# Kernel tuning notes

Hardware: AMD Instinct MI355X
Metric: run time of the kernel (lower is better)

Reference implementation:

```python
import jax, jax.numpy as jnp
import numpy as np

B, S, D, H = 4, 2048, 1024, 16
DH = D // H


def setup_inputs() -> dict:
    key = jax.random.key(0)
    ks = jax.random.split(key, 5)
    scale = 0.02
    return {
        "in_features": jax.random.normal(ks[0], (B, S, D), dtype=jnp.float32),
        "Wq": jax.random.normal(ks[1], (D, D), dtype=jnp.float32) * scale,
        "Wk": jax.random.normal(ks[2], (D, D), dtype=jnp.float32) * scale,
        "Wv": jax.random.normal(ks[3], (D, D), dtype=jnp.float32) * scale,
        "Wo": jax.random.normal(ks[4], (D, D), dtype=jnp.float32) * scale,
    }


def reference(in_features, Wq, Wk, Wv, Wo):
    x = in_features  # [B, S, D]
    # projections: einsum '... s d_in, d_model d_in -> ... s d_model'  == x @ W.T
    q = jnp.einsum('bsd,md->bsm', x, Wq)
    k = jnp.einsum('bsd,md->bsm', x, Wk)
    v = jnp.einsum('bsd,md->bsm', x, Wv)
    # split heads: [B, H, S, DH]
    q = q.reshape(B, S, H, DH).transpose(0, 2, 1, 3)
    k = k.reshape(B, S, H, DH).transpose(0, 2, 1, 3)
    v = v.reshape(B, S, H, DH).transpose(0, 2, 1, 3)
    scale = 1.0 / jnp.sqrt(jnp.asarray(DH, dtype=q.dtype))
    scores = jnp.einsum('bhqd,bhkd->bhqk', q, k) * scale  # [B, H, S, S]
    causal = jnp.tril(jnp.ones((S, S), dtype=bool))
    scores = jnp.where(causal[None, None, :, :], scores, -jnp.inf)
    attn = jax.nn.softmax(scores, axis=-1)
    out = jnp.einsum('bhqk,bhkd->bhqd', attn, v)  # [B, H, S, DH]
    out = out.transpose(0, 2, 1, 3).reshape(B, S, D)
    # output projection: einsum '... s d_v, d_model d_v -> ... s d_model' == out @ Wo.T
    return jnp.einsum('bsd,md->bsm', out, Wo)
```

## Files before the change

### kernel.cpp

```cpp
#include <hip/hip_runtime.h>

typedef unsigned short u16;
typedef __attribute__((ext_vector_type(8))) short bf16x8;
typedef __attribute__((ext_vector_type(4))) short bf16x4;
typedef __attribute__((ext_vector_type(4))) float f32x4;

#define S_LEN 2048
#define NHEAD 16
#define DHEAD 64
#define DMODEL 1024

__device__ __forceinline__ u16 f2bf(float f) {
  unsigned u = __builtin_bit_cast(unsigned, f);
  unsigned r = (u + 0x7fffu + ((u >> 16) & 1u)) >> 16;
  return (u16)r;
}

__device__ __forceinline__ void gld_lds16(const void* g, void* l) {
  __builtin_amdgcn_global_load_lds((const __attribute__((address_space(1))) unsigned*)g,
                                   (__attribute__((address_space(3))) unsigned*)l,
                                   16, 0, 0);
}

__global__ void cast_bf16_kernel(const float* __restrict__ in, u16* __restrict__ out, int n4) {
  int i = blockIdx.x * 256 + threadIdx.x;
  if (i >= n4) return;
  float4 v = reinterpret_cast<const float4*>(in)[i];
  ushort4 o;
  o.x = f2bf(v.x); o.y = f2bf(v.y); o.z = f2bf(v.z); o.w = f2bf(v.w);
  reinterpret_cast<ushort4*>(out)[i] = o;
}

__global__ void cast_w_kernel(const float* __restrict__ Wq, const float* __restrict__ Wk,
                              const float* __restrict__ Wv, const float* __restrict__ Wo,
                              u16* __restrict__ out) {
  int id = blockIdx.x * 256 + threadIdx.x;
  int wsel = id >> 18, j = id & 262143;
  const float* s = wsel < 2 ? (wsel == 0 ? Wq : Wk) : (wsel == 2 ? Wv : Wo);
  float4 v = reinterpret_cast<const float4*>(s)[j];
  ushort4 o;
  o.x = f2bf(v.x); o.y = f2bf(v.y); o.z = f2bf(v.z); o.w = f2bf(v.w);
  reinterpret_cast<ushort4*>(out)[id] = o;
}

__global__ __launch_bounds__(256) void gemm_bt(const u16* __restrict__ A, const u16* __restrict__ Bw,
                                               void* __restrict__ outp, int mode) {
  __shared__ u16 lA[2][128 * 32];
  __shared__ u16 lB[2][128 * 32];
  const int hw = blockIdx.x;
  const int xcd = hw & 7, vv = hw >> 3;
  const int bx = vv >> 3, by = xcd * 8 + (vv & 7);
  const int tid = threadIdx.x;
  const int w = tid >> 6, lane = tid & 63;
  const int wm = w >> 1, wn = w & 1;
  const int c = lane & 15, qr = lane >> 4;
  const int brow = by * 128, bcol = bx * 128;
  f32x4 acc[4][4];
#pragma unroll
  for (int m = 0; m < 4; ++m)
#pragma unroll
    for (int n = 0; n < 4; ++n) acc[m][n] = (f32x4){0.f, 0.f, 0.f, 0.f};

  auto stage = [&](int kt, int bsel) {
    const int k0 = kt * 32;
#pragma unroll
    for (int i = 0; i < 2; ++i) {
      int slot = i * 256 + w * 64 + lane;
      int r = slot >> 2, sg = slot & 3;
      gld_lds16(A + (size_t)(brow + r) * DMODEL + k0 + sg * 8, &lA[bsel][(i * 256 + w * 64) * 8]);
      gld_lds16(Bw + (size_t)(bcol + r) * DMODEL + k0 + sg * 8, &lB[bsel][(i * 256 + w * 64) * 8]);
    }
  };

  stage(0, 0);
  __syncthreads();
  int cur = 0;
  for (int kt = 0; kt < 32; ++kt) {
    if (kt < 31) stage(kt + 1, cur ^ 1);
    bf16x8 af[4], bfr[4];
#pragma unroll
    for (int m = 0; m < 4; ++m) af[m] = *(const bf16x8*)(&lA[cur][(wm * 64 + m * 16 + c) * 32 + qr * 8]);
#pragma unroll
    for (int n = 0; n < 4; ++n) bfr[n] = *(const bf16x8*)(&lB[cur][(wn * 64 + n * 16 + c) * 32 + qr * 8]);
    __builtin_amdgcn_s_setprio(1);
#pragma unroll
    for (int m = 0; m < 4; ++m)
#pragma unroll
      for (int n = 0; n < 4; ++n)
        acc[m][n] = __builtin_amdgcn_mfma_f32_16x16x32_bf16(af[m], bfr[n], acc[m][n], 0, 0, 0);
    __builtin_amdgcn_s_setprio(0);
    __syncthreads();
    cur ^= 1;
  }

  const int rb = qr * 4;
#pragma unroll
  for (int m = 0; m < 4; ++m) {
#pragma unroll
    for (int n = 0; n < 4; ++n) {
      f32x4 a = acc[m][n];
      int gm0 = brow + wm * 64 + m * 16 + rb;
      int gn = bcol + wn * 64 + n * 16 + c;
      if (mode == 3) {
        float* op = (float*)outp;
#pragma unroll
        for (int r = 0; r < 4; ++r) op[(size_t)(gm0 + r) * DMODEL + gn] = a[r];
      } else {
        u16* Qb = (u16*)outp;
        u16* Kb = Qb + 8388608;
        u16* Vt = Kb + 8388608;
        int mat = gn >> 10, gl = gn & 1023;
        int hh = gl >> 6, dh = gl & 63;
        int b = gm0 >> 11;
        if (mat == 2) {
          int s0 = gm0 & 2047;
          ushort4 pk;
          pk.x = f2bf(a[0]); pk.y = f2bf(a[1]); pk.z = f2bf(a[2]); pk.w = f2bf(a[3]);
          *reinterpret_cast<ushort4*>(Vt + ((size_t)(b * NHEAD + hh) * DHEAD + dh) * S_LEN + (s0)) = pk;
        } else {
          float scale = (mat == 0) ? 0.1803368801111204f : 1.0f;
          u16* dst = (mat == 0) ? Qb : Kb;
#pragma unroll
          for (int r = 0; r < 4; ++r) {
            int gm = gm0 + r;
            int s = gm & 2047;
            dst[((size_t)(b * NHEAD + hh) * S_LEN + s) * DHEAD + dh] = f2bf(a[r] * scale);
          }
        }
      }
    }
  }
}

__global__ __launch_bounds__(512, 4) void attn_kernel(const u16* __restrict__ Q, const u16* __restrict__ K,
                                                      const u16* __restrict__ Vt, u16* __restrict__ O) {
  __shared__ u16 lsK[2][64 * 64];
  __shared__ u16 lsV[2][64 * 64];
  __shared__ u16 lsP[8][16 * 64];
  const int hw = blockIdx.x;
  const int xcd = hw & 7, vv = hw >> 3;
  const int by = xcd * 8 + (vv >> 3);
  const int j = vv & 7;
  const int tid = threadIdx.x;
  const int w = tid >> 6, lane = tid & 63;
  const int c = lane & 15, qr = lane >> 4;
  const int b = by >> 4, h = by & 15;
  u16* lp = lsP[w];

  const int q0A = j * 128 + w * 16;
  const int q0B = (15 - j) * 128 + w * 16;
  const int ndA = q0A >> 6, ndB = q0B >> 6;
  const int ntiles = 32 - 2 * j;

  const u16* qra = Q + ((size_t)by * S_LEN + q0A + c) * DHEAD;
  const u16* qrb = Q + ((size_t)by * S_LEN + q0B + c) * DHEAD;
  const bf16x8 aQA0 = *(const bf16x8*)(qra + qr * 8);
  const bf16x8 aQA1 = *(const bf16x8*)(qra + 32 + qr * 8);
  const bf16x8 aQB0 = *(const bf16x8*)(qrb + qr * 8);
  const bf16x8 aQB1 = *(const bf16x8*)(qrb + 32 + qr * 8);

  f32x4 oA[4], oB[4];
#pragma unroll
  for (int d = 0; d < 4; ++d) { oA[d] = (f32x4){0.f, 0.f, 0.f, 0.f}; oB[d] = oA[d]; }
  float mA = -1e30f, lA_ = 0.f, mB = -1e30f, lB_ = 0.f;

  auto stage = [&](int kt, int bsel) {
    const int kv0 = kt * 64;
    int r = tid >> 3, p = tid & 7;
    int ps = p ^ (r & 7);
    gld_lds16(K + ((size_t)by * S_LEN + kv0 + r) * DHEAD + ps * 8, &lsK[bsel][(w * 64) * 8]);
    gld_lds16(Vt + ((size_t)by * DHEAD + r) * S_LEN + kv0 + ps * 8, &lsV[bsel][(w * 64) * 8]);
  };

  auto process = [&](const u16* bK, const u16* bV, int kt, int nd, int q0,
                     const bf16x8& aQ0, const bf16x8& aQ1,
                     f32x4* o_acc, float& m_run, float& l_run) {
    const int kv0 = kt * 64;
    f32x4 sc[4];
    __builtin_amdgcn_s_setprio(1);
#pragma unroll
    for (int nt = 0; nt < 4; ++nt) {
      int row = nt * 16 + c;
      const bf16x8 k0 = *(const bf16x8*)(bK + row * 64 + ((qr ^ (row & 7)) * 8));
      const bf16x8 k1 = *(const bf16x8*)(bK + row * 64 + (((4 + qr) ^ (row & 7)) * 8));
      f32x4 z = (f32x4){0.f, 0.f, 0.f, 0.f};
      z = __builtin_amdgcn_mfma_f32_16x16x32_bf16(k0, aQ0, z, 0, 0, 0);
      z = __builtin_amdgcn_mfma_f32_16x16x32_bf16(k1, aQ1, z, 0, 0, 0);
      sc[nt] = z;
    }
    __builtin_amdgcn_s_setprio(0);

    if (kt == nd) {
#pragma unroll
      for (int nt = 0; nt < 4; ++nt)
#pragma unroll
        for (int r = 0; r < 4; ++r) {
          int k_g = kv0 + nt * 16 + qr * 4 + r;
          int q_g = q0 + c;
          if (k_g > q_g) sc[nt][r] = -1e30f;
        }
    }

    float tm = fmaxf(fmaxf(fmaxf(sc[0][0], sc[0][1]), fmaxf(sc[0][2], sc[0][3])),
                     fmaxf(fmaxf(sc[1][0], sc[1][1]), fmaxf(sc[1][2], sc[1][3])));
    tm = fmaxf(tm, fmaxf(fmaxf(fmaxf(sc[2][0], sc[2][1]), fmaxf(sc[2][2], sc[2][3])),
                         fmaxf(fmaxf(sc[3][0], sc[3][1]), fmaxf(sc[3][2], sc[3][3]))));
    tm = fmaxf(tm, __shfl_xor(tm, 16));
    tm = fmaxf(tm, __shfl_xor(tm, 32));
    if (tm > m_run + 11.5f) {
      float al = __builtin_amdgcn_exp2f(m_run - tm);
      l_run *= al;
#pragma unroll
      for (int dt = 0; dt < 4; ++dt)
#pragma unroll
        for (int r = 0; r < 4; ++r) o_acc[dt][r] *= al;
      m_run = tm;
    }
    float rs = 0.f;
#pragma unroll
    for (int nt = 0; nt < 4; ++nt) {
      ushort4 pk;
#pragma unroll
      for (int r = 0; r < 4; ++r) {
        float p = __builtin_amdgcn_exp2f(sc[nt][r] - m_run);
        rs += p;
        ((u16*)&pk)[r] = f2bf(p);
      }
      *reinterpret_cast<ushort4*>(lp + c * 64 + (((nt * 4 + qr) ^ c) * 4)) = pk;
    }
    rs += __shfl_xor(rs, 16);
    rs += __shfl_xor(rs, 32);
    l_run += rs;

    bf16x8 pb[2];
#pragma unroll
    for (int ks = 0; ks < 2; ++ks) {
      bf16x4 lo = *(const bf16x4*)(lp + c * 64 + (((ks * 8 + qr * 2) ^ c) * 4));
      bf16x4 hi = *(const bf16x4*)(lp + c * 64 + (((ks * 8 + qr * 2 + 1) ^ c) * 4));
      pb[ks] = (bf16x8){lo[0], lo[1], lo[2], lo[3], hi[0], hi[1], hi[2], hi[3]};
    }
    __builtin_amdgcn_s_setprio(1);
#pragma unroll
    for (int dt = 0; dt < 4; ++dt) {
      int rowv = dt * 16 + c;
#pragma unroll
      for (int ks = 0; ks < 2; ++ks) {
        const bf16x8 vb = *(const bf16x8*)(bV + rowv * 64 + (((ks * 4 + qr) ^ (rowv & 7)) * 8));
        o_acc[dt] = __builtin_amdgcn_mfma_f32_16x16x32_bf16(vb, pb[ks], o_acc[dt], 0, 0, 0);
      }
    }
    __builtin_amdgcn_s_setprio(0);
  };

  stage(0, 0);
  __syncthreads();
  int cur = 0;
  for (int kt = 0; kt < ntiles; ++kt) {
    if (kt + 1 < ntiles) stage(kt + 1, cur ^ 1);
    if (kt <= ndB) process(lsK[cur], lsV[cur], kt, ndB, q0B, aQB0, aQB1, oB, mB, lB_);
    if (kt <= ndA) process(lsK[cur], lsV[cur], kt, ndA, q0A, aQA0, aQA1, oA, mA, lA_);
    __syncthreads();
    cur ^= 1;
  }

  {
    float rl = 1.0f / lB_;
    int s = q0B + c;
#pragma unroll
    for (int dt = 0; dt < 4; ++dt) {
      ushort4 ok;
#pragma unroll
      for (int r = 0; r < 4; ++r) ((u16*)&ok)[r] = f2bf(oB[dt][r] * rl);
      *reinterpret_cast<ushort4*>(O + (((size_t)b * S_LEN + s) * NHEAD + h) * DHEAD + dt * 16 + qr * 4) = ok;
    }
  }
  {
    float rl = 1.0f / lA_;
    int s = q0A + c;
#pragma unroll
    for (int dt = 0; dt < 4; ++dt) {
      ushort4 ok;
#pragma unroll
      for (int r = 0; r < 4; ++r) ((u16*)&ok)[r] = f2bf(oA[dt][r] * rl);
      *reinterpret_cast<ushort4*>(O + (((size_t)b * S_LEN + s) * NHEAD + h) * DHEAD + dt * 16 + qr * 4) = ok;
    }
  }
}

extern "C" void kernel_launch(void* const* d_in, const int* in_sizes, int n_in,
                              void* d_out, int out_size, void* d_ws, size_t ws_size,
                              hipStream_t stream) {
  (void)in_sizes; (void)n_in; (void)out_size; (void)ws_size;
  const float* x  = (const float*)d_in[0];
  const float* Wq = (const float*)d_in[1];
  const float* Wk = (const float*)d_in[2];
  const float* Wv = (const float*)d_in[3];
  const float* Wo = (const float*)d_in[4];

  u16* ws  = (u16*)d_ws;
  u16* xb  = ws;
  u16* wqb = xb  + 8388608;
  u16* wob = wqb + 3145728;
  u16* Qb  = wqb + 4194304;
  u16* Kb  = Qb  + 8388608;
  u16* Vt  = Kb  + 8388608;
  u16* Ob  = Vt  + 8388608;

  cast_bf16_kernel<<<8192, 256, 0, stream>>>(x, xb, 2097152);
  cast_w_kernel<<<4096, 256, 0, stream>>>(Wq, Wk, Wv, Wo, wqb);

  gemm_bt<<<1536, 256, 0, stream>>>(xb, wqb, Qb, 4);
  attn_kernel<<<512, 512, 0, stream>>>(Qb, Kb, Vt, Ob);
  gemm_bt<<<512, 256, 0, stream>>>(Ob, wob, (void*)d_out, 3);
}
```

Baseline: 188.5 us.

## Add 256x256 pipelined QKV GEMM kernel and tweak attention inner loop

Replaces the QKV projection GEMM with a new 512-thread kernel that computes 256x256 tiles with a K-step of 64. It uses a double-buffered global_load_lds pipeline, explicit vmcnt waits and barrier-separated MFMA quarter phases to overlap loads with matrix math. The attention kernel now packs probabilities to bf16 by truncation via perm instead of round-to-nearest, and its K/V loop is unrolled by two so buffer indices are constants. The output GEMM is specialised to fp32 output. The risks are slightly different bf16 rounding of P, higher register pressure, and an odd tile count if ntiles were odd.

```diff
diff --git a/kernel.cpp b/kernel.cpp
--- a/kernel.cpp
+++ b/kernel.cpp
@@ -1,6 +1,7 @@
 #include <hip/hip_runtime.h>
 
 typedef unsigned short u16;
+typedef unsigned int u32;
 typedef __attribute__((ext_vector_type(8))) short bf16x8;
 typedef __attribute__((ext_vector_type(4))) short bf16x4;
 typedef __attribute__((ext_vector_type(4))) float f32x4;
@@ -43,8 +44,154 @@
   reinterpret_cast<ushort4*>(out)[id] = o;
 }
 
+#define MFMA_Q(mlo, nlo)                                                                     \
+  _Pragma("unroll") for (int m_ = 0; m_ < 4; ++m_)                                           \
+  _Pragma("unroll") for (int n_ = 0; n_ < 2; ++n_)                                           \
+  _Pragma("unroll") for (int kk_ = 0; kk_ < 2; ++kk_)                                        \
+    acc[(mlo) + m_][(nlo) + n_] = __builtin_amdgcn_mfma_f32_16x16x32_bf16(                   \
+        af[(mlo) + m_][kk_], bf[(nlo) + n_][kk_], acc[(mlo) + m_][(nlo) + n_], 0, 0, 0);
+
+#define VM6 do { __builtin_amdgcn_sched_barrier(0);                                          \
+  asm volatile("s_waitcnt vmcnt(6)" ::: "memory");                                           \
+  __builtin_amdgcn_sched_barrier(0); } while (0)
+#define VM0 do { __builtin_amdgcn_sched_barrier(0);                                          \
+  asm volatile("s_waitcnt vmcnt(0)" ::: "memory");                                           \
+  __builtin_amdgcn_sched_barrier(0); } while (0)
+
+#define HALF_ITER(bb, S1, S2, S3, S4, WAIT) do {                                             \
+  const u16* aB = aB0 + (bb)*32768;                                                          \
+  const u16* bB = bB0 + (bb)*32768;                                                          \
+                                                                                     \
+  _Pragma("unroll") for (int m_ = 0; m_ < 4; ++m_) {                                         \
+    af[m_][0] = rdA(aB, m_, 0); af[m_][1] = rdA(aB, m_, 1); }                                \
+  _Pragma("unroll") for (int n_ = 0; n_ < 2; ++n_) {                                         \
+    bf[n_][0] = rdB(bB, n_, 0); bf[n_][1] = rdB(bB, n_, 1); }                                \
+  S1;                                                                                        \
+  __builtin_amdgcn_s_barrier();                                                              \
+  __builtin_amdgcn_s_setprio(1); MFMA_Q(0, 0) __builtin_amdgcn_s_setprio(0);                 \
+  __builtin_amdgcn_s_barrier();                                                              \
+                                                                                     \
+  _Pragma("unroll") for (int m_ = 0; m_ < 4; ++m_) {                                         \
+    af[4 + m_][0] = rdA(aB, 4 + m_, 0); af[4 + m_][1] = rdA(aB, 4 + m_, 1); }                \
+  S2;                                                                                        \
+  __builtin_amdgcn_s_barrier();                                                              \
+  __builtin_amdgcn_s_setprio(1); MFMA_Q(4, 0) __builtin_amdgcn_s_setprio(0);                 \
+  __builtin_amdgcn_s_barrier();                                                              \
+                                                                                     \
+  _Pragma("unroll") for (int n_ = 0; n_ < 2; ++n_) {                                         \
+    bf[2 + n_][0] = rdB(bB, 2 + n_, 0); bf[2 + n_][1] = rdB(bB, 2 + n_, 1); }                \
+  S3;                                                                                        \
+  __builtin_amdgcn_s_barrier();                                                              \
+  __builtin_amdgcn_s_setprio(1); MFMA_Q(0, 2) __builtin_amdgcn_s_setprio(0);                 \
+  __builtin_amdgcn_s_barrier();                                                              \
+                                                                                     \
+  S4;                                                                                        \
+  __builtin_amdgcn_s_barrier();                                                              \
+  __builtin_amdgcn_s_setprio(1); MFMA_Q(4, 2) __builtin_amdgcn_s_setprio(0);                 \
+  WAIT;                                                                                      \
+  __builtin_amdgcn_s_barrier();                                                              \
+} while (0)
+
+__global__ __launch_bounds__(512, 2) void gemm_qkv(const u16* __restrict__ A,
+                                                   const u16* __restrict__ Bw,
+                                                   u16* __restrict__ Qb) {
+  __shared__ u16 lds[65536];
+  const int bid = blockIdx.x;
+  const int xcd = bid & 7, v = bid >> 3;
+  const int by = xcd * 4 + (v & 3), bx = v >> 2;
+  const int brow = by * 256, bcol = bx * 256;
+  const int tid = threadIdx.x;
+  const int w = tid >> 6, lane = tid & 63;
+  const int wm = w >> 2, wn = w & 3;
+  const int c = lane & 15, qr = lane >> 4;
+  const int sq = (qr * 8) ^ (((c >> 2) & 1) << 4);
+
+  auto stg = [&](int mat, int tau, int half) {
+    if (tau >= 16) return;
+    u16* region = lds + (tau & 1) * 32768 + mat * 16384 + half * 8192;
+    const u16* G = mat ? Bw : A;
+    int rowb = (mat ? bcol : brow) + half * 128;
+    int k0 = tau * 64;
+#pragma unroll
+    for (int i = 0; i < 2; ++i) {
+      int slot = i * 512 + tid;
+      int r = slot >> 3, cb = slot & 7;
+      int cbs = cb ^ (((r >> 2) & 1) << 1);
+      gld_lds16(G + (size_t)(rowb + r) * DMODEL + k0 + cbs * 8, region + (i * 512 + w * 64) * 8);
+    }
+  };
+
+  auto rdA = [&](const u16* base, int m, int kk) {
+    return *(const bf16x8*)(base + (m * 16 + c) * 64 + kk * 32 + sq);
+  };
+  auto rdB = [&](const u16* base, int n, int kk) {
+    return *(const bf16x8*)(base + ((wn & 1) * 64 + n * 16 + c) * 64 + kk * 32 + sq);
+  };
+
+  f32x4 acc[8][4];
+#pragma unroll
+  for (int m = 0; m < 8; ++m)
+#pragma unroll
+    for (int n = 0; n < 4; ++n) acc[m][n] = (f32x4){0.f, 0.f, 0.f, 0.f};
+  bf16x8 af[8][2], bf[4][2];
+  const u16* aB0 = lds + wm * 8192;
+  const u16* bB0 = lds + 16384 + (wn >> 1) * 8192;
+
+  stg(0, 0, 0); stg(0, 0, 1); stg(1, 0, 0); stg(1, 0, 1);
+  stg(0, 1, 0); stg(0, 1, 1); stg(1, 1, 0);
+  VM6;
+  __builtin_amdgcn_s_barrier();
+
+#pragma unroll 1
+  for (int t = 0; t < 8; ++t) {
+    const int e = 2 * t;
+    HALF_ITER(0,
+              stg(1, e + 1, 1),
+              stg(0, e + 2, 0),
+              stg(0, e + 2, 1),
+              stg(1, e + 2, 0),
+              if (t < 7) { VM6; } else { VM0; });
+    HALF_ITER(1,
+              stg(1, e + 2, 1),
+              stg(0, e + 3, 0),
+              stg(0, e + 3, 1),
+              stg(1, e + 3, 0),
+              if (t < 7) { VM6; });
+  }
+
+  u16* Kb = Qb + 8388608;
+  u16* Vt = Kb + 8388608;
+#pragma unroll
+  for (int m = 0; m < 8; ++m) {
+#pragma unroll
+    for (int n = 0; n < 4; ++n) {
+      f32x4 a = acc[m][n];
+      int gm0 = brow + wm * 128 + m * 16 + qr * 4;
+      int gn = bcol + wn * 64 + n * 16 + c;
+      int mat = gn >> 10, gl = gn & 1023;
+      int hh = gl >> 6, dh = gl & 63;
+      int b = gm0 >> 11;
+      if (mat == 2) {
+        int s0 = gm0 & 2047;
+        ushort4 pk;
+        pk.x = f2bf(a[0]); pk.y = f2bf(a[1]); pk.z = f2bf(a[2]); pk.w = f2bf(a[3]);
+        *reinterpret_cast<ushort4*>(Vt + ((size_t)(b * NHEAD + hh) * DHEAD + dh) * S_LEN + s0) = pk;
+      } else {
+        float scale = (mat == 0) ? 0.1803368801111204f : 1.0f;
+        u16* dst = (mat == 0) ? Qb : Kb;
+#pragma unroll
+        for (int r = 0; r < 4; ++r) {
+          int gm = gm0 + r;
+          int s = gm & 2047;
+          dst[((size_t)(b * NHEAD + hh) * S_LEN + s) * DHEAD + dh] = f2bf(a[r] * scale);
+        }
+      }
+    }
+  }
+}
+
 __global__ __launch_bounds__(256) void gemm_bt(const u16* __restrict__ A, const u16* __restrict__ Bw,
-                                               void* __restrict__ outp, int mode) {
+                                               float* __restrict__ outp) {
   __shared__ u16 lA[2][128 * 32];
   __shared__ u16 lB[2][128 * 32];
   const int hw = blockIdx.x;
@@ -95,41 +242,15 @@
 
   const int rb = qr * 4;
 #pragma unroll
-  for (int m = 0; m < 4; ++m) {
+  for (int m = 0; m < 4; ++m)
 #pragma unroll
     for (int n = 0; n < 4; ++n) {
       f32x4 a = acc[m][n];
       int gm0 = brow + wm * 64 + m * 16 + rb;
       int gn = bcol + wn * 64 + n * 16 + c;
-      if (mode == 3) {
-        float* op = (float*)outp;
-#pragma unroll
-        for (int r = 0; r < 4; ++r) op[(size_t)(gm0 + r) * DMODEL + gn] = a[r];
-      } else {
-        u16* Qb = (u16*)outp;
-        u16* Kb = Qb + 8388608;
-        u16* Vt = Kb + 8388608;
-        int mat = gn >> 10, gl = gn & 1023;
-        int hh = gl >> 6, dh = gl & 63;
-        int b = gm0 >> 11;
-        if (mat == 2) {
-          int s0 = gm0 & 2047;
-          ushort4 pk;
-          pk.x = f2bf(a[0]); pk.y = f2bf(a[1]); pk.z = f2bf(a[2]); pk.w = f2bf(a[3]);
-          *reinterpret_cast<ushort4*>(Vt + ((size_t)(b * NHEAD + hh) * DHEAD + dh) * S_LEN + (s0)) = pk;
-        } else {
-          float scale = (mat == 0) ? 0.1803368801111204f : 1.0f;
-          u16* dst = (mat == 0) ? Qb : Kb;
-#pragma unroll
-          for (int r = 0; r < 4; ++r) {
-            int gm = gm0 + r;
-            int s = gm & 2047;
-            dst[((size_t)(b * NHEAD + hh) * S_LEN + s) * DHEAD + dh] = f2bf(a[r] * scale);
-          }
-        }
-      }
-    }
-  }
+#pragma unroll
+      for (int r = 0; r < 4; ++r) outp[(size_t)(gm0 + r) * DMODEL + gn] = a[r];
+    }
 }
 
 __global__ __launch_bounds__(512, 4) void attn_kernel(const u16* __restrict__ Q, const u16* __restrict__ K,
@@ -219,14 +340,15 @@
     float rs = 0.f;
 #pragma unroll
     for (int nt = 0; nt < 4; ++nt) {
-      ushort4 pk;
-#pragma unroll
-      for (int r = 0; r < 4; ++r) {
-        float p = __builtin_amdgcn_exp2f(sc[nt][r] - m_run);
-        rs += p;
-        ((u16*)&pk)[r] = f2bf(p);
-      }
-      *reinterpret_cast<ushort4*>(lp + c * 64 + (((nt * 4 + qr) ^ c) * 4)) = pk;
+      float p0 = __builtin_amdgcn_exp2f(sc[nt][0] - m_run);
+      float p1 = __builtin_amdgcn_exp2f(sc[nt][1] - m_run);
+      float p2 = __builtin_amdgcn_exp2f(sc[nt][2] - m_run);
+      float p3 = __builtin_amdgcn_exp2f(sc[nt][3] - m_run);
+      rs += (p0 + p1) + (p2 + p3);
+      u32 w01 = __builtin_amdgcn_perm(__builtin_bit_cast(u32, p1), __builtin_bit_cast(u32, p0), 0x07060302u);
+      u32 w23 = __builtin_amdgcn_perm(__builtin_bit_cast(u32, p3), __builtin_bit_cast(u32, p2), 0x07060302u);
+      uint2 pk; pk.x = w01; pk.y = w23;
+      *reinterpret_cast<uint2*>(lp + c * 64 + (((nt * 4 + qr) ^ c) * 4)) = pk;
     }
     rs += __shfl_xor(rs, 16);
     rs += __shfl_xor(rs, 32);
@@ -254,13 +376,16 @@
 
   stage(0, 0);
   __syncthreads();
-  int cur = 0;
-  for (int kt = 0; kt < ntiles; ++kt) {
-    if (kt + 1 < ntiles) stage(kt + 1, cur ^ 1);
-    if (kt <= ndB) process(lsK[cur], lsV[cur], kt, ndB, q0B, aQB0, aQB1, oB, mB, lB_);
-    if (kt <= ndA) process(lsK[cur], lsV[cur], kt, ndA, q0A, aQA0, aQA1, oA, mA, lA_);
+  for (int kt = 0; kt < ntiles; kt += 2) {
+    if (kt + 1 < ntiles) stage(kt + 1, 1);
+    if (kt <= ndB) process(lsK[0], lsV[0], kt, ndB, q0B, aQB0, aQB1, oB, mB, lB_);
+    if (kt <= ndA) process(lsK[0], lsV[0], kt, ndA, q0A, aQA0, aQA1, oA, mA, lA_);
     __syncthreads();
-    cur ^= 1;
+    const int k2 = kt + 1;
+    if (k2 + 1 < ntiles) stage(k2 + 1, 0);
+    if (k2 <= ndB) process(lsK[1], lsV[1], k2, ndB, q0B, aQB0, aQB1, oB, mB, lB_);
+    if (k2 <= ndA) process(lsK[1], lsV[1], k2, ndA, q0A, aQA0, aQA1, oA, mA, lA_);
+    __syncthreads();
   }
 
   {
@@ -309,7 +434,7 @@
   cast_bf16_kernel<<<8192, 256, 0, stream>>>(x, xb, 2097152);
   cast_w_kernel<<<4096, 256, 0, stream>>>(Wq, Wk, Wv, Wo, wqb);
 
-  gemm_bt<<<1536, 256, 0, stream>>>(xb, wqb, Qb, 4);
+  gemm_qkv<<<384, 512, 0, stream>>>(xb, wqb, Qb);
   attn_kernel<<<512, 512, 0, stream>>>(Qb, Kb, Vt, Ob);
-  gemm_bt<<<512, 256, 0, stream>>>(Ob, wob, (void*)d_out, 3);
-}
+  gemm_bt<<<512, 256, 0, stream>>>(Ob, wob, (float*)d_out);
+}
```

After: 183.6 us. 2.6% less time.
